# Kernel tuning notes

Hardware: AMD Instinct MI355X
Metric: run time of the kernel (lower is better)

Reference implementation:

```python
import jax, jax.numpy as jnp
import numpy as np

B = 256          # batch; loop count == len(x) == B
I = 1024         # input_size
H = 1024         # hidden_size
OUT = 2


def setup_inputs() -> dict:
    key = jax.random.key(0)
    ks = jax.random.split(key, 7)
    s_ih = 1.0 / np.sqrt(H)
    return {
        "x": jax.random.normal(ks[0], (B, B, I), dtype=jnp.float32),
        "hidden": jnp.zeros((B, H), dtype=jnp.float32),
        "W_ih": jax.random.uniform(ks[1], (H, I), jnp.float32, -s_ih, s_ih),
        "b_ih": jax.random.uniform(ks[2], (H,), jnp.float32, -s_ih, s_ih),
        "W_hh": jax.random.uniform(ks[3], (H, H), jnp.float32, -s_ih, s_ih),
        "b_hh": jax.random.uniform(ks[4], (H,), jnp.float32, -s_ih, s_ih),
        "fc_w": jax.random.uniform(ks[5], (OUT, H), jnp.float32, -s_ih, s_ih),
        "fc_b": jax.random.uniform(ks[6], (OUT,), jnp.float32, -s_ih, s_ih),
    }


def reference(x, hidden, W_ih, b_ih, W_hh, b_hh, fc_w, fc_b):
    nb = x.shape[0]
    # torch loop: for idx in range(len(x)): hidden = rnncell(x[:, idx], hidden)
    # -> scan over the first len(x) timesteps along dim 1
    xs = jnp.swapaxes(x, 0, 1)[:nb]  # [T=B, B, I]

    def step(h, xt):
        h_new = jnp.tanh(xt @ W_ih.T + b_ih + h @ W_hh.T + b_hh)
        return h_new, h_new

    h_last, hs = jax.lax.scan(step, hidden, xs)  # hs: [T, B, H]
    # torch.cat along dim0 -> [T*B, H]; reshape(len(x), -1, H) with T==B gives
    # indexing [t, b, h]; output[:, -1] selects the last batch element per step.
    last = hs[:, -1, :]            # [T, H]
    out = last @ fc_w.T + fc_b     # [T, 2]
    return out, h_last
```

## Files before the change

kernel.cpp:

```cpp
#include <hip/hip_runtime.h>
#include <math.h>

#define TS 256
#define NB 256
#define HD 1024
#define ID 1024

typedef __attribute__((ext_vector_type(8))) short bf16x8;
typedef __attribute__((ext_vector_type(4))) float f32x4;

__device__ __forceinline__ void splitf(float x, int& hi, int& lo) {
  union { float f; unsigned u; } a; a.f = x;
  unsigned t = a.u + 0x7FFFu + ((a.u >> 16) & 1u);
  unsigned hb = t & 0xFFFF0000u;
  union { unsigned u; float f; } hf; hf.u = hb;
  float lf = x - hf.f;
  union { float f; unsigned u; } b; b.f = lf;
  unsigned t2 = b.u + 0x7FFFu + ((b.u >> 16) & 1u);
  hi = (int)(t >> 16);
  lo = (int)(t2 >> 16);
}

__global__ __launch_bounds__(256) void k_split(
    const float* __restrict__ src, short* __restrict__ dhi,
    short* __restrict__ dlo, int n4)
{
  int i = blockIdx.x * 256 + threadIdx.x;
  if (i >= n4) return;
  float4 v = ((const float4*)src)[i];
  int h0, h1, h2, h3, l0, l1, l2, l3;
  splitf(v.x, h0, l0); splitf(v.y, h1, l1);
  splitf(v.z, h2, l2); splitf(v.w, h3, l3);
  ((int2*)dhi)[i] = make_int2((h0 & 0xFFFF) | (h1 << 16), (h2 & 0xFFFF) | (h3 << 16));
  ((int2*)dlo)[i] = make_int2((l0 & 0xFFFF) | (l1 << 16), (l2 & 0xFFFF) | (l3 << 16));
}

__global__ __launch_bounds__(256) void k_precompute(
    const float* __restrict__ x, const float* __restrict__ Wih,
    const float* __restrict__ bih, const float* __restrict__ bhh,
    float* __restrict__ A, int t0)
{
  __shared__ float As[32][68];
  __shared__ float Bs[32][68];
  const int tid = threadIdx.x;
  const int tx = tid & 15, ty = tid >> 4;
  const int c0 = blockIdx.x * 64;
  const int m0 = blockIdx.y * 64;
  const int t_local = m0 >> 8;
  const int t = t0 + t_local;

  float acc[4][4] = {};

  for (int k0 = 0; k0 < ID; k0 += 32) {
    #pragma unroll
    for (int l = 0; l < 2; ++l) {
      int v = tid + l * 256;
      int r = v >> 3, kq = v & 7;
      int b = (m0 + r) & 255;
      const float4 val = *(const float4*)(x + (size_t)b * TS * ID
                                            + (size_t)t * ID + k0 + kq * 4);
      As[kq*4+0][r] = val.x; As[kq*4+1][r] = val.y;
      As[kq*4+2][r] = val.z; As[kq*4+3][r] = val.w;
    }
    #pragma unroll
    for (int l = 0; l < 2; ++l) {
      int v = tid + l * 256;
      int c = v >> 3, kq = v & 7;
      const float4 val = *(const float4*)(Wih + (size_t)(c0 + c) * ID + k0 + kq * 4);
      Bs[kq*4+0][c] = val.x; Bs[kq*4+1][c] = val.y;
      Bs[kq*4+2][c] = val.z; Bs[kq*4+3][c] = val.w;
    }
    __syncthreads();
    #pragma unroll
    for (int kk = 0; kk < 32; ++kk) {
      float a0 = As[kk][ty*4+0], a1 = As[kk][ty*4+1];
      float a2 = As[kk][ty*4+2], a3 = As[kk][ty*4+3];
      float b0 = Bs[kk][tx*4+0], b1 = Bs[kk][tx*4+1];
      float b2 = Bs[kk][tx*4+2], b3 = Bs[kk][tx*4+3];
      acc[0][0] += a0*b0; acc[0][1] += a0*b1; acc[0][2] += a0*b2; acc[0][3] += a0*b3;
      acc[1][0] += a1*b0; acc[1][1] += a1*b1; acc[1][2] += a1*b2; acc[1][3] += a1*b3;
      acc[2][0] += a2*b0; acc[2][1] += a2*b1; acc[2][2] += a2*b2; acc[2][3] += a2*b3;
      acc[3][0] += a3*b0; acc[3][1] += a3*b1; acc[3][2] += a3*b2; acc[3][3] += a3*b3;
    }
    __syncthreads();
  }
  #pragma unroll
  for (int i = 0; i < 4; ++i) {
    int m = m0 + ty * 4 + i;
    #pragma unroll
    for (int j = 0; j < 4; ++j) {
      int c = c0 + tx * 4 + j;
      A[(size_t)m * HD + c] = acc[i][j] + bih[c] + bhh[c];
    }
  }
}

__global__ __launch_bounds__(256) void k_step(
    const short* __restrict__ hhi_in, const short* __restrict__ hlo_in,
    const short* __restrict__ whi, const short* __restrict__ wlo,
    const float* __restrict__ Azt,
    short* __restrict__ hhi_out, short* __restrict__ hlo_out,
    float* __restrict__ hf32, float* __restrict__ last_t)
{
  __shared__ float4 HsHi[2][512];
  __shared__ float4 HsLo[2][512];
  __shared__ float4 WsHi[2][512];
  __shared__ float4 WsLo[2][512];

  const int tid = threadIdx.x;
  const int n0 = blockIdx.x * 32;
  const int m0 = blockIdx.y * 32;
  const int l  = tid & 63;
  const int wv = tid >> 6;
  const int wm = wv >> 1, wn = wv & 1;
  const int fr = l & 15, fg = l >> 4;
  const int rowA = wm * 16 + fr;
  const int rowB = wn * 16 + fr;
  const int swA = rowA & 7, swB = rowB & 7;

  f32x4 acc = {0.f, 0.f, 0.f, 0.f};

  #define STAGE(d, k0)                                                        \
    {                                                                         \
      _Pragma("unroll")                                                       \
      for (int hf = 0; hf < 2; ++hf) {                                        \
        int c = tid + hf * 256;                                               \
        int row = c >> 4, c16 = c & 15;                                       \
        int dst = row * 16 + (c16 ^ (row & 7));                               \
        size_t soH = (size_t)(m0 + row) * HD + (k0) + c16 * 8;                \
        size_t soW = (size_t)(n0 + row) * HD + (k0) + c16 * 8;                \
        HsHi[d][dst] = *(const float4*)(hhi_in + soH);                        \
        HsLo[d][dst] = *(const float4*)(hlo_in + soH);                        \
        WsHi[d][dst] = *(const float4*)(whi + soW);                           \
        WsLo[d][dst] = *(const float4*)(wlo + soW);                           \
      }                                                                       \
    }

  STAGE(0, 0)
  __syncthreads();

  for (int r = 0; r < 8; ++r) {
    const int d = r & 1;
    if (r < 7) STAGE(d ^ 1, (r + 1) * 128)
    #pragma unroll
    for (int ks = 0; ks < 4; ++ks) {
      const int ku = ks * 4 + fg;
      bf16x8 ahi = *(const bf16x8*)&HsHi[d][rowA * 16 + (ku ^ swA)];
      bf16x8 alo = *(const bf16x8*)&HsLo[d][rowA * 16 + (ku ^ swA)];
      bf16x8 bhi = *(const bf16x8*)&WsHi[d][rowB * 16 + (ku ^ swB)];
      bf16x8 blo = *(const bf16x8*)&WsLo[d][rowB * 16 + (ku ^ swB)];
      acc = __builtin_amdgcn_mfma_f32_16x16x32_bf16(ahi, bhi, acc, 0, 0, 0);
      acc = __builtin_amdgcn_mfma_f32_16x16x32_bf16(ahi, blo, acc, 0, 0, 0);
      acc = __builtin_amdgcn_mfma_f32_16x16x32_bf16(alo, bhi, acc, 0, 0, 0);
      acc = __builtin_amdgcn_mfma_f32_16x16x32_bf16(alo, blo, acc, 0, 0, 0);
    }
    __syncthreads();
  }

  const int col = n0 + wn * 16 + fr;
  #pragma unroll
  for (int g = 0; g < 4; ++g) {
    int m = m0 + wm * 16 + fg * 4 + g;
    float z = acc[g] + Azt[(size_t)m * HD + col];
    float hv = tanhf(z);
    hf32[(size_t)m * HD + col] = hv;
    int hi, lo; splitf(hv, hi, lo);
    hhi_out[(size_t)m * HD + col] = (short)hi;
    hlo_out[(size_t)m * HD + col] = (short)lo;
    if (m == NB - 1) last_t[col] = hv;
  }
}

__global__ __launch_bounds__(256) void k_out(
    const float* __restrict__ last, const float* __restrict__ fcw,
    const float* __restrict__ fcb, float* __restrict__ out)
{
  const int t = blockIdx.x, tid = threadIdx.x;
  float s0 = 0.f, s1 = 0.f;
  for (int j = tid; j < HD; j += 256) {
    float v = last[(size_t)t * HD + j];
    s0 += v * fcw[j];
    s1 += v * fcw[HD + j];
  }
  #pragma unroll
  for (int off = 32; off > 0; off >>= 1) {
    s0 += __shfl_down(s0, off);
    s1 += __shfl_down(s1, off);
  }
  __shared__ float r0[4], r1[4];
  int w = tid >> 6;
  if ((tid & 63) == 0) { r0[w] = s0; r1[w] = s1; }
  __syncthreads();
  if (tid == 0) {
    out[t * 2 + 0] = r0[0] + r0[1] + r0[2] + r0[3] + fcb[0];
    out[t * 2 + 1] = r1[0] + r1[1] + r1[2] + r1[3] + fcb[1];
  }
}

extern "C" void kernel_launch(void* const* d_in, const int* in_sizes, int n_in,
                              void* d_out, int out_size, void* d_ws, size_t ws_size,
                              hipStream_t stream)
{
  const float* x   = (const float*)d_in[0];
  const float* h0  = (const float*)d_in[1];
  const float* Wih = (const float*)d_in[2];
  const float* bih = (const float*)d_in[3];
  const float* Whh = (const float*)d_in[4];
  const float* bhh = (const float*)d_in[5];
  const float* fcw = (const float*)d_in[6];
  const float* fcb = (const float*)d_in[7];
  float* out = (float*)d_out;

  float* h    = (float*)d_ws;
  float* last = h + (size_t)NB * HD;
  short* whi  = (short*)(last + (size_t)TS * HD);
  short* wlo  = whi + (size_t)HD * HD;
  short* hhi0 = wlo + (size_t)HD * HD;
  short* hlo0 = hhi0 + (size_t)NB * HD;
  short* hhi1 = hlo0 + (size_t)NB * HD;
  short* hlo1 = hhi1 + (size_t)NB * HD;
  float* A    = (float*)(hlo1 + (size_t)NB * HD);

  const size_t per_t = (size_t)NB * HD * sizeof(float);
  const size_t fixed = (size_t)(A - (float*)d_ws) * sizeof(float);
  int chunkT = TS;
  if (ws_size < fixed + (size_t)TS * per_t) {
    long long avail = (long long)ws_size - (long long)fixed;
    chunkT = (int)(avail / (long long)per_t);
    if (chunkT < 1) chunkT = 1;
    if (chunkT > TS) chunkT = TS;
  }

  k_split<<<dim3((HD * HD / 4 + 255) / 256), 256, 0, stream>>>(Whh, whi, wlo, HD * HD / 4);
  k_split<<<dim3((NB * HD / 4 + 255) / 256), 256, 0, stream>>>(h0, hhi0, hlo0, NB * HD / 4);

  short* hhi[2] = {hhi0, hhi1};
  short* hlo[2] = {hlo0, hlo1};
  int cur = 0;

  for (int t0 = 0; t0 < TS; t0 += chunkT) {
    const int ct = (chunkT < TS - t0) ? chunkT : (TS - t0);
    dim3 g1(HD / 64, ct * 4);
    k_precompute<<<g1, 256, 0, stream>>>(x, Wih, bih, bhh, A, t0);
    for (int tl = 0; tl < ct; ++tl) {
      float* zt = A + (size_t)tl * NB * HD;
      k_step<<<dim3(HD / 32, NB / 32), 256, 0, stream>>>(
          hhi[cur], hlo[cur], whi, wlo, zt,
          hhi[cur ^ 1], hlo[cur ^ 1], h, last + (size_t)(t0 + tl) * HD);
      cur ^= 1;
    }
  }
  k_out<<<TS, 256, 0, stream>>>(last, fcw, fcb, out);
  hipMemcpyAsync(out + TS * 2, h, per_t, hipMemcpyDeviceToDevice, stream);
}
```

Baseline: 5.000 ms.

## Fuse recurrent steps into persistent cooperative kernel and move input GEMM to MFMA

Replaces the 256 per-timestep launches with one cooperative persistent kernel. Each of its 256 blocks keeps its W_hh slice resident in shared memory and waits on per-row-group flag barriers between timesteps. The input projection GEMM moves from scalar FP32 FMAs to split-bf16 MFMA with 3 products and 128x128 tiles, with W_ih pre-split on device. This removes launch overhead and repeated W_hh reloads, at the cost of spin-wait barriers, a cooperative-launch requirement, and slightly lower precision in the input projection.

```diff
diff --git a/kernel.cpp b/kernel.cpp
--- a/kernel.cpp
+++ b/kernel.cpp
@@ -35,139 +35,205 @@
   ((int2*)dlo)[i] = make_int2((l0 & 0xFFFF) | (l1 << 16), (l2 & 0xFFFF) | (l3 << 16));
 }
 
-__global__ __launch_bounds__(256) void k_precompute(
-    const float* __restrict__ x, const float* __restrict__ Wih,
+__global__ __launch_bounds__(256) void k_gemm_pre(
+    const float* __restrict__ x,
+    const short* __restrict__ wih_hi, const short* __restrict__ wih_lo,
     const float* __restrict__ bih, const float* __restrict__ bhh,
     float* __restrict__ A, int t0)
 {
-  __shared__ float As[32][68];
-  __shared__ float Bs[32][68];
+  __shared__ uint4 sXh[1024], sXl[1024], sWh[1024], sWl[1024];
+
   const int tid = threadIdx.x;
-  const int tx = tid & 15, ty = tid >> 4;
-  const int c0 = blockIdx.x * 64;
-  const int m0 = blockIdx.y * 64;
-  const int t_local = m0 >> 8;
-  const int t = t0 + t_local;
-
-  float acc[4][4] = {};
-
-  for (int k0 = 0; k0 < ID; k0 += 32) {
-    #pragma unroll
-    for (int l = 0; l < 2; ++l) {
-      int v = tid + l * 256;
-      int r = v >> 3, kq = v & 7;
-      int b = (m0 + r) & 255;
-      const float4 val = *(const float4*)(x + (size_t)b * TS * ID
-                                            + (size_t)t * ID + k0 + kq * 4);
-      As[kq*4+0][r] = val.x; As[kq*4+1][r] = val.y;
-      As[kq*4+2][r] = val.z; As[kq*4+3][r] = val.w;
-    }
-    #pragma unroll
-    for (int l = 0; l < 2; ++l) {
-      int v = tid + l * 256;
-      int c = v >> 3, kq = v & 7;
-      const float4 val = *(const float4*)(Wih + (size_t)(c0 + c) * ID + k0 + kq * 4);
-      Bs[kq*4+0][c] = val.x; Bs[kq*4+1][c] = val.y;
-      Bs[kq*4+2][c] = val.z; Bs[kq*4+3][c] = val.w;
-    }
-    __syncthreads();
-    #pragma unroll
-    for (int kk = 0; kk < 32; ++kk) {
-      float a0 = As[kk][ty*4+0], a1 = As[kk][ty*4+1];
-      float a2 = As[kk][ty*4+2], a3 = As[kk][ty*4+3];
-      float b0 = Bs[kk][tx*4+0], b1 = Bs[kk][tx*4+1];
-      float b2 = Bs[kk][tx*4+2], b3 = Bs[kk][tx*4+3];
-      acc[0][0] += a0*b0; acc[0][1] += a0*b1; acc[0][2] += a0*b2; acc[0][3] += a0*b3;
-      acc[1][0] += a1*b0; acc[1][1] += a1*b1; acc[1][2] += a1*b2; acc[1][3] += a1*b3;
-      acc[2][0] += a2*b0; acc[2][1] += a2*b1; acc[2][2] += a2*b2; acc[2][3] += a2*b3;
-      acc[3][0] += a3*b0; acc[3][1] += a3*b1; acc[3][2] += a3*b2; acc[3][3] += a3*b3;
-    }
-    __syncthreads();
-  }
-  #pragma unroll
-  for (int i = 0; i < 4; ++i) {
-    int m = m0 + ty * 4 + i;
-    #pragma unroll
-    for (int j = 0; j < 4; ++j) {
-      int c = c0 + tx * 4 + j;
-      A[(size_t)m * HD + c] = acc[i][j] + bih[c] + bhh[c];
-    }
-  }
-}
-
-__global__ __launch_bounds__(256) void k_step(
-    const short* __restrict__ hhi_in, const short* __restrict__ hlo_in,
-    const short* __restrict__ whi, const short* __restrict__ wlo,
-    const float* __restrict__ Azt,
-    short* __restrict__ hhi_out, short* __restrict__ hlo_out,
-    float* __restrict__ hf32, float* __restrict__ last_t)
-{
-  __shared__ float4 HsHi[2][512];
-  __shared__ float4 HsLo[2][512];
-  __shared__ float4 WsHi[2][512];
-  __shared__ float4 WsLo[2][512];
-
-  const int tid = threadIdx.x;
-  const int n0 = blockIdx.x * 32;
-  const int m0 = blockIdx.y * 32;
-  const int l  = tid & 63;
-  const int wv = tid >> 6;
+  const int bid = blockIdx.x;
+  const int nb  = bid & 7;
+  const int mbi = bid >> 3;
+  const int tl  = mbi >> 1;
+  const int b0  = (mbi & 1) * 128;
+  const int t   = t0 + tl;
+  const int n0  = nb * 128;
+
+  const int l  = tid & 63, wv = tid >> 6;
   const int wm = wv >> 1, wn = wv & 1;
   const int fr = l & 15, fg = l >> 4;
-  const int rowA = wm * 16 + fr;
-  const int rowB = wn * 16 + fr;
-  const int swA = rowA & 7, swB = rowB & 7;
-
-  f32x4 acc = {0.f, 0.f, 0.f, 0.f};
-
-  #define STAGE(d, k0)                                                        \
-    {                                                                         \
-      _Pragma("unroll")                                                       \
-      for (int hf = 0; hf < 2; ++hf) {                                        \
-        int c = tid + hf * 256;                                               \
-        int row = c >> 4, c16 = c & 15;                                       \
-        int dst = row * 16 + (c16 ^ (row & 7));                               \
-        size_t soH = (size_t)(m0 + row) * HD + (k0) + c16 * 8;                \
-        size_t soW = (size_t)(n0 + row) * HD + (k0) + c16 * 8;                \
-        HsHi[d][dst] = *(const float4*)(hhi_in + soH);                        \
-        HsLo[d][dst] = *(const float4*)(hlo_in + soH);                        \
-        WsHi[d][dst] = *(const float4*)(whi + soW);                           \
-        WsLo[d][dst] = *(const float4*)(wlo + soW);                           \
-      }                                                                       \
-    }
-
-  STAGE(0, 0)
+
+  f32x4 acc[4][4] = {};
+
+  for (int k0 = 0; k0 < ID; k0 += 64) {
+    #pragma unroll
+    for (int i = 0; i < 4; ++i) {
+      int v = tid + i * 256;
+      int row = v >> 3, u = v & 7;
+      const float* gp = x + ((size_t)(b0 + row) * TS + t) * ID + k0 + u * 8;
+      float4 v0 = *(const float4*)gp;
+      float4 v1 = *(const float4*)(gp + 4);
+      int h0,h1,h2,h3,h4,h5,h6,h7, q0,q1,q2,q3,q4,q5,q6,q7;
+      splitf(v0.x,h0,q0); splitf(v0.y,h1,q1); splitf(v0.z,h2,q2); splitf(v0.w,h3,q3);
+      splitf(v1.x,h4,q4); splitf(v1.y,h5,q5); splitf(v1.z,h6,q6); splitf(v1.w,h7,q7);
+      uint4 ph, pl;
+      ph.x=(h0&0xFFFF)|(h1<<16); ph.y=(h2&0xFFFF)|(h3<<16);
+      ph.z=(h4&0xFFFF)|(h5<<16); ph.w=(h6&0xFFFF)|(h7<<16);
+      pl.x=(q0&0xFFFF)|(q1<<16); pl.y=(q2&0xFFFF)|(q3<<16);
+      pl.z=(q4&0xFFFF)|(q5<<16); pl.w=(q6&0xFFFF)|(q7<<16);
+      int dst = row * 8 + (u ^ (row & 7));
+      sXh[dst] = ph; sXl[dst] = pl;
+    }
+    #pragma unroll
+    for (int i = 0; i < 4; ++i) {
+      int v = tid + i * 256;
+      int row = v >> 3, u = v & 7;
+      size_t so = (size_t)(n0 + row) * ID + k0 + u * 8;
+      int dst = row * 8 + (u ^ (row & 7));
+      sWh[dst] = *(const uint4*)(wih_hi + so);
+      sWl[dst] = *(const uint4*)(wih_lo + so);
+    }
+    __syncthreads();
+
+    #pragma unroll
+    for (int ku = 0; ku < 2; ++ku) {
+      bf16x8 xh[4], xl[4], wh[4], wl[4];
+      #pragma unroll
+      for (int i = 0; i < 4; ++i) {
+        int rA = wm * 64 + i * 16 + fr;
+        int uA = (ku * 4 + fg) ^ (rA & 7);
+        xh[i] = *(const bf16x8*)&sXh[rA * 8 + uA];
+        xl[i] = *(const bf16x8*)&sXl[rA * 8 + uA];
+        int rB = wn * 64 + i * 16 + fr;
+        int uB = (ku * 4 + fg) ^ (rB & 7);
+        wh[i] = *(const bf16x8*)&sWh[rB * 8 + uB];
+        wl[i] = *(const bf16x8*)&sWl[rB * 8 + uB];
+      }
+      #pragma unroll
+      for (int mt = 0; mt < 4; ++mt)
+        #pragma unroll
+        for (int nt = 0; nt < 4; ++nt) {
+          acc[mt][nt] = __builtin_amdgcn_mfma_f32_16x16x32_bf16(xh[mt], wh[nt], acc[mt][nt], 0,0,0);
+          acc[mt][nt] = __builtin_amdgcn_mfma_f32_16x16x32_bf16(xl[mt], wh[nt], acc[mt][nt], 0,0,0);
+          acc[mt][nt] = __builtin_amdgcn_mfma_f32_16x16x32_bf16(xh[mt], wl[nt], acc[mt][nt], 0,0,0);
+        }
+    }
+    __syncthreads();
+  }
+
+  #pragma unroll
+  for (int nt = 0; nt < 4; ++nt) {
+    int col = n0 + wn * 64 + nt * 16 + fr;
+    float bsum = bih[col] + bhh[col];
+    #pragma unroll
+    for (int mt = 0; mt < 4; ++mt)
+      #pragma unroll
+      for (int g = 0; g < 4; ++g) {
+        int mloc = wm * 64 + mt * 16 + fg * 4 + g;
+        A[((size_t)tl * NB + b0 + mloc) * HD + col] = acc[mt][nt][g] + bsum;
+      }
+  }
+}
+
+__global__ __launch_bounds__(256) void k_steps(
+    const short* __restrict__ whh_hi, const short* __restrict__ whh_lo,
+    const float* __restrict__ A,
+    short* __restrict__ hh0, short* __restrict__ hl0,
+    short* __restrict__ hh1, short* __restrict__ hl1,
+    float* __restrict__ hf32, float* __restrict__ last,
+    int* __restrict__ flags, int t0, int ct, int cur0)
+{
+  __shared__ uint4 sWh[4096];
+  __shared__ uint4 sWl[4096];
+
+  const int tid = threadIdx.x;
+  const int bid = blockIdx.x;
+  const int nb  = bid & 31;
+  const int mb  = bid >> 5;
+  const int l   = tid & 63, wv = tid >> 6;
+  const int wm  = wv >> 1, wn = wv & 1;
+  const int fr  = l & 15, fg = l >> 4;
+
+  for (int i = 0; i < 16; ++i) {
+    int v = tid + i * 256;
+    int row = v >> 7, u = v & 127;
+    int dst = row * 128 + (u ^ (row & 7));
+    size_t so = (size_t)(nb * 32 + row) * HD + u * 8;
+    sWh[dst] = *(const uint4*)(whh_hi + so);
+    sWl[dst] = *(const uint4*)(whh_lo + so);
+  }
   __syncthreads();
 
-  for (int r = 0; r < 8; ++r) {
-    const int d = r & 1;
-    if (r < 7) STAGE(d ^ 1, (r + 1) * 128)
-    #pragma unroll
-    for (int ks = 0; ks < 4; ++ks) {
-      const int ku = ks * 4 + fg;
-      bf16x8 ahi = *(const bf16x8*)&HsHi[d][rowA * 16 + (ku ^ swA)];
-      bf16x8 alo = *(const bf16x8*)&HsLo[d][rowA * 16 + (ku ^ swA)];
-      bf16x8 bhi = *(const bf16x8*)&WsHi[d][rowB * 16 + (ku ^ swB)];
-      bf16x8 blo = *(const bf16x8*)&WsLo[d][rowB * 16 + (ku ^ swB)];
-      acc = __builtin_amdgcn_mfma_f32_16x16x32_bf16(ahi, bhi, acc, 0, 0, 0);
-      acc = __builtin_amdgcn_mfma_f32_16x16x32_bf16(ahi, blo, acc, 0, 0, 0);
-      acc = __builtin_amdgcn_mfma_f32_16x16x32_bf16(alo, bhi, acc, 0, 0, 0);
-      acc = __builtin_amdgcn_mfma_f32_16x16x32_bf16(alo, blo, acc, 0, 0, 0);
-    }
+  const int rowH = mb * 32 + wm * 16 + fr;
+  const int rowW = wn * 16 + fr;
+  const int sw   = rowW & 7;
+  const int colC = nb * 32 + wn * 16 + fr;
+  const int mrow0 = mb * 32 + wm * 16 + fg * 4;
+
+  int cur = cur0;
+  for (int tl = 0; tl < ct; ++tl) {
+    const int t = t0 + tl;
+    const short* ghi = cur ? hh1 : hh0;
+    const short* glo = cur ? hl1 : hl0;
+    short* ohi = cur ? hh0 : hh1;
+    short* olo = cur ? hl0 : hl1;
+    const float* At = A + (size_t)tl * NB * HD;
+
+    float aval[4];
+    #pragma unroll
+    for (int g = 0; g < 4; ++g)
+      aval[g] = At[(size_t)(mrow0 + g) * HD + colC];
+
+    const short* pH = ghi + (size_t)rowH * HD + fg * 8;
+    const short* pL = glo + (size_t)rowH * HD + fg * 8;
+
+    f32x4 acc = {0.f, 0.f, 0.f, 0.f};
+    bf16x8 fh[3][4], fl[3][4];
+
+    #define LOADG(s, g)                                                     \
+      { _Pragma("unroll")                                                   \
+        for (int j = 0; j < 4; ++j) {                                       \
+          int ku = (g) * 4 + j;                                             \
+          fh[s][j] = *(const bf16x8*)(pH + ku * 32);                        \
+          fl[s][j] = *(const bf16x8*)(pL + ku * 32);                        \
+        } }
+
+    LOADG(0, 0)
+    LOADG(1, 1)
+    #pragma unroll
+    for (int grp = 0; grp < 8; ++grp) {
+      const int sc = grp % 3, s2 = (grp + 2) % 3;
+      if (grp < 6) LOADG(s2, grp + 2)
+      #pragma unroll
+      for (int j = 0; j < 4; ++j) {
+        int ku = grp * 4 + j;
+        int un = (ku * 4 + fg) ^ sw;
+        bf16x8 bh = *(const bf16x8*)&sWh[rowW * 128 + un];
+        bf16x8 bl = *(const bf16x8*)&sWl[rowW * 128 + un];
+        acc = __builtin_amdgcn_mfma_f32_16x16x32_bf16(fh[sc][j], bh, acc, 0,0,0);
+        acc = __builtin_amdgcn_mfma_f32_16x16x32_bf16(fh[sc][j], bl, acc, 0,0,0);
+        acc = __builtin_amdgcn_mfma_f32_16x16x32_bf16(fl[sc][j], bh, acc, 0,0,0);
+        acc = __builtin_amdgcn_mfma_f32_16x16x32_bf16(fl[sc][j], bl, acc, 0,0,0);
+      }
+    }
+    #undef LOADG
+
+    #pragma unroll
+    for (int g = 0; g < 4; ++g) {
+      int m = mrow0 + g;
+      float hv = tanhf(acc[g] + aval[g]);
+      int hi_, lo_; splitf(hv, hi_, lo_);
+      size_t off = (size_t)m * HD + colC;
+      ohi[off] = (short)hi_;
+      olo[off] = (short)lo_;
+      if (t == TS - 1) hf32[off] = hv;
+      if (m == NB - 1) last[(size_t)t * HD + colC] = hv;
+    }
+
+    __threadfence();
     __syncthreads();
-  }
-
-  const int col = n0 + wn * 16 + fr;
-  #pragma unroll
-  for (int g = 0; g < 4; ++g) {
-    int m = m0 + wm * 16 + fg * 4 + g;
-    float z = acc[g] + Azt[(size_t)m * HD + col];
-    float hv = tanhf(z);
-    hf32[(size_t)m * HD + col] = hv;
-    int hi, lo; splitf(hv, hi, lo);
-    hhi_out[(size_t)m * HD + col] = (short)hi;
-    hlo_out[(size_t)m * HD + col] = (short)lo;
-    if (m == NB - 1) last_t[col] = hv;
+    if (tid == 0) {
+      int fi = t * 8 + mb;
+      __hip_atomic_fetch_add(&flags[fi], 1, __ATOMIC_RELEASE, __HIP_MEMORY_SCOPE_AGENT);
+      while (__hip_atomic_load(&flags[fi], __ATOMIC_RELAXED, __HIP_MEMORY_SCOPE_AGENT) < 32)
+        __builtin_amdgcn_s_sleep(2);
+    }
+    __syncthreads();
+    __threadfence();
+    cur ^= 1;
   }
 }
 
@@ -206,23 +272,26 @@
   const float* Wih = (const float*)d_in[2];
   const float* bih = (const float*)d_in[3];
   const float* Whh = (const float*)d_in[4];
+  const float* fcw = (const float*)d_in[6];
   const float* bhh = (const float*)d_in[5];
-  const float* fcw = (const float*)d_in[6];
   const float* fcb = (const float*)d_in[7];
   float* out = (float*)d_out;
 
   float* h    = (float*)d_ws;
   float* last = h + (size_t)NB * HD;
-  short* whi  = (short*)(last + (size_t)TS * HD);
-  short* wlo  = whi + (size_t)HD * HD;
-  short* hhi0 = wlo + (size_t)HD * HD;
-  short* hlo0 = hhi0 + (size_t)NB * HD;
-  short* hhi1 = hlo0 + (size_t)NB * HD;
-  short* hlo1 = hhi1 + (size_t)NB * HD;
-  float* A    = (float*)(hlo1 + (size_t)NB * HD);
+  short* whhh = (short*)(last + (size_t)TS * HD);
+  short* whhl = whhh + (size_t)HD * HD;
+  short* wihh = whhl + (size_t)HD * HD;
+  short* wihl = wihh + (size_t)HD * HD;
+  short* hh0  = wihl + (size_t)HD * HD;
+  short* hl0  = hh0 + (size_t)NB * HD;
+  short* hh1  = hl0 + (size_t)NB * HD;
+  short* hl1  = hh1 + (size_t)NB * HD;
+  int*   flags= (int*)(hl1 + (size_t)NB * HD);
+  float* A    = (float*)(flags + TS * 8);
 
   const size_t per_t = (size_t)NB * HD * sizeof(float);
-  const size_t fixed = (size_t)(A - (float*)d_ws) * sizeof(float);
+  const size_t fixed = (size_t)((char*)A - (char*)d_ws);
   int chunkT = TS;
   if (ws_size < fixed + (size_t)TS * per_t) {
     long long avail = (long long)ws_size - (long long)fixed;
@@ -231,24 +300,23 @@
     if (chunkT > TS) chunkT = TS;
   }
 
-  k_split<<<dim3((HD * HD / 4 + 255) / 256), 256, 0, stream>>>(Whh, whi, wlo, HD * HD / 4);
-  k_split<<<dim3((NB * HD / 4 + 255) / 256), 256, 0, stream>>>(h0, hhi0, hlo0, NB * HD / 4);
-
-  short* hhi[2] = {hhi0, hhi1};
-  short* hlo[2] = {hlo0, hlo1};
+  hipMemsetAsync(flags, 0, TS * 8 * sizeof(int), stream);
+  k_split<<<dim3(HD * HD / 4 / 256), 256, 0, stream>>>(Whh, whhh, whhl, HD * HD / 4);
+  k_split<<<dim3(HD * HD / 4 / 256), 256, 0, stream>>>(Wih, wihh, wihl, HD * HD / 4);
+  k_split<<<dim3(NB * HD / 4 / 256), 256, 0, stream>>>(h0, hh0, hl0, NB * HD / 4);
+
   int cur = 0;
-
   for (int t0 = 0; t0 < TS; t0 += chunkT) {
     const int ct = (chunkT < TS - t0) ? chunkT : (TS - t0);
-    dim3 g1(HD / 64, ct * 4);
-    k_precompute<<<g1, 256, 0, stream>>>(x, Wih, bih, bhh, A, t0);
-    for (int tl = 0; tl < ct; ++tl) {
-      float* zt = A + (size_t)tl * NB * HD;
-      k_step<<<dim3(HD / 32, NB / 32), 256, 0, stream>>>(
-          hhi[cur], hlo[cur], whi, wlo, zt,
-          hhi[cur ^ 1], hlo[cur ^ 1], h, last + (size_t)(t0 + tl) * HD);
-      cur ^= 1;
-    }
+    k_gemm_pre<<<dim3(ct * 16), 256, 0, stream>>>(x, wihh, wihl, bih, bhh, A, t0);
+    void* args[] = {
+      (void*)&whhh, (void*)&whhl, (void*)&A,
+      (void*)&hh0, (void*)&hl0, (void*)&hh1, (void*)&hl1,
+      (void*)&h, (void*)&last, (void*)&flags,
+      (void*)&t0, (void*)&ct, (void*)&cur
+    };
+    hipLaunchCooperativeKernel((void*)k_steps, dim3(256), dim3(256), args, 0, stream);
+    cur ^= (ct & 1);
   }
   k_out<<<TS, 256, 0, stream>>>(last, fcw, fcb, out);
   hipMemcpyAsync(out + TS * 2, h, per_t, hipMemcpyDeviceToDevice, stream);
```

Result: slower. 18.60 ms (+272.0%).
